# Kernel tuning notes

Measured on AMD Instinct MI355X. Metric: run time of the kernel, lower is better.

## Reference

```python
import jax, jax.numpy as jnp
import numpy as np
from jax.scipy.special import logsumexp

EPS = 0.05        # sinkhorn entropic blur (geomloss default blur=0.05, p=1 -> eps=blur)
N_ITERS = 10      # fixed sinkhorn iterations
A_W, B_W = 1.0, 1.0  # chamfer / EMD weights (c=0: projectionLoss undefined in source)


def setup_inputs() -> dict:
    key = jax.random.key(0)
    k1, k2 = jax.random.split(key)
    output = jax.random.normal(k1, (16, 2048, 3), dtype=jnp.float32)
    target = jax.random.normal(k2, (16, 2048, 3), dtype=jnp.float32)
    return {"output": output, "target": target}


def _pairwise_sqdist(x, y):
    # x: [B,N,3], y: [B,M,3] -> [B,N,M]
    x2 = jnp.sum(x * x, axis=-1)                      # [B,N]
    y2 = jnp.sum(y * y, axis=-1)                      # [B,M]
    xy = jnp.einsum('bnd,bmd->bnm', x, y)             # [B,N,M]
    return jnp.maximum(x2[:, :, None] + y2[:, None, :] - 2.0 * xy, 1e-12)


def _total_loss(output, target):
    B, N, _ = output.shape
    M = target.shape[1]
    d2 = _pairwise_sqdist(output, target)             # [B,N,M]

    # Chamfer distance: sum of min squared distances in both directions
    chamfer = jnp.sum(jnp.min(d2, axis=2)) + jnp.sum(jnp.min(d2, axis=1))

    # Sinkhorn EMD with p=1 cost (L2 distance), uniform weights, log-domain
    C = jnp.sqrt(d2)                                  # [B,N,M]
    log_mu = jnp.full((B, N), -jnp.log(jnp.float32(N)), dtype=C.dtype)
    log_nu = jnp.full((B, M), -jnp.log(jnp.float32(M)), dtype=C.dtype)
    f = jnp.zeros((B, N), dtype=C.dtype)
    g = jnp.zeros((B, M), dtype=C.dtype)

    def body(carry, _):
        f, g = carry
        # g_j = -eps * LSE_i[(f_i - C_ij)/eps + log_mu_i]
        g = -EPS * logsumexp((f[:, :, None] - C) / EPS + log_mu[:, :, None], axis=1)
        # f_i = -eps * LSE_j[(g_j - C_ij)/eps + log_nu_j]
        f = -EPS * logsumexp((g[:, None, :] - C) / EPS + log_nu[:, None, :], axis=2)
        return (f, g), None

    (f, g), _ = jax.lax.scan(body, (f, g), None, length=N_ITERS)
    mu = jnp.exp(log_mu)
    nu = jnp.exp(log_nu)
    emd = jnp.sum(mu * f, axis=1) + jnp.sum(nu * g, axis=1)   # [B] dual objective
    emd_loss = jnp.sum(emd * jnp.float32(N))

    return A_W * chamfer + B_W * emd_loss


def reference(output, target):
    return _total_loss(output, target)
```

## Files before the change

kernel.cpp:

```cpp
#include <hip/hip_runtime.h>
#include <math.h>

#define NPTS    2048
#define NBATCH  16
#define THREADS 256
#define BLOCKS_PER_BATCH 64
#define ROWS_PER_BLOCK   32
#define ROWS_PER_WAVE    8
#define IPAIRS  1024

typedef __attribute__((ext_vector_type(2))) float f2;

static constexpr float KEPS_L  = 28.853900817779268f;
static constexpr float LOGMU_L = -11.0f;
static constexpr float EPS_LN2 = 0.03465735902799727f;
static constexpr float INV_K2  = 1.2011331562368226e-3f;

__global__ void pack_pts(const float* __restrict__ a, const float* __restrict__ b,
                         float4* __restrict__ pa, float4* __restrict__ pb) {
  int idx = blockIdx.x * blockDim.x + threadIdx.x;
  if (idx < NBATCH * NPTS) {
    float x = KEPS_L * a[3*idx], y = KEPS_L * a[3*idx+1], z = KEPS_L * a[3*idx+2];
    pa[idx] = make_float4(x, y, z, fmaf(x, x, fmaf(y, y, z*z)));
    float u = KEPS_L * b[3*idx], v = KEPS_L * b[3*idx+1], w = KEPS_L * b[3*idx+2];
    pb[idx] = make_float4(u, v, w, fmaf(u, u, fmaf(v, v, w*w)));
  }
}

template<bool INIT, bool CHAMFER>
__global__ __launch_bounds__(THREADS)
void lse_pass(const float4* __restrict__ pR, const float4* __restrict__ pQ,
              const float* __restrict__ dualR, float* __restrict__ dualQ,
              float* __restrict__ chamPart) {
  __shared__ f2 sxx[IPAIRS];
  __shared__ f2 syy[IPAIRS];
  __shared__ f2 szz[IPAIRS];
  __shared__ f2 sww[IPAIRS];
  __shared__ f2 swt[IPAIRS];

  const int b    = blockIdx.x >> 6;
  const int blk  = blockIdx.x & 63;
  const int tid  = threadIdx.x;
  const int lane = tid & 63;
  const int wave = tid >> 6;

  const float4* __restrict__ px = pR + b * NPTS;
  float A;

  if constexpr (INIT) {
#pragma unroll
    for (int u = 0; u < 4; ++u) {
      int k = tid + u * THREADS;
      float4 a4 = px[k];
      float4 b4 = px[k + IPAIRS];
      sxx[k] = (f2){a4.x, b4.x};
      syy[k] = (f2){a4.y, b4.y};
      szz[k] = (f2){a4.z, b4.z};
      sww[k] = (f2){-0.5f * a4.w, -0.5f * b4.w};
      swt[k] = (f2){1.f, 1.f};
    }
    A = LOGMU_L;
    __syncthreads();
  } else {
    const float* __restrict__ fb = dualR + b * NPTS;
    float av[8];
    float lm = -3.4e38f;
#pragma unroll
    for (int u = 0; u < 8; ++u) {
      int k = tid + u * THREADS;
      float a = fmaf(fb[k], KEPS_L, LOGMU_L);
      av[u] = a;
      lm = fmaxf(lm, a);
    }
#pragma unroll
    for (int off = 32; off; off >>= 1) lm = fmaxf(lm, __shfl_xor(lm, off));
    float* scratch = (float*)sxx;
    if (lane == 0) scratch[wave] = lm;
    __syncthreads();
    A = fmaxf(fmaxf(scratch[0], scratch[1]), fmaxf(scratch[2], scratch[3]));
    __syncthreads();
#pragma unroll
    for (int u = 0; u < 4; ++u) {
      int k = tid + u * THREADS;
      float4 a4 = px[k];
      float4 b4 = px[k + IPAIRS];
      sxx[k] = (f2){a4.x, b4.x};
      syy[k] = (f2){a4.y, b4.y};
      szz[k] = (f2){a4.z, b4.z};
      sww[k] = (f2){-0.5f * a4.w, -0.5f * b4.w};
      swt[k] = (f2){__builtin_amdgcn_exp2f(av[u] - A),
                    __builtin_amdgcn_exp2f(av[u + 4] - A)};
    }
    __syncthreads();
  }

  const float4* __restrict__ qa = pQ + b * NPTS;
  float* __restrict__ gout = dualQ + b * NPTS;
  const int j0 = blk * ROWS_PER_BLOCK + wave * ROWS_PER_WAVE;

  f2 qxx[8], qyy[8], qzz[8], qww[8], s2[8], m2[8];
#pragma unroll
  for (int r = 0; r < ROWS_PER_WAVE; ++r) {
    float4 q = qa[j0 + r];
    qxx[r] = (f2){q.x, q.x};
    qyy[r] = (f2){q.y, q.y};
    qzz[r] = (f2){q.z, q.z};
    qww[r] = (f2){q.w, q.w};
    s2[r] = (f2){0.f, 0.f};
    if constexpr (CHAMFER) m2[r] = (f2){3.4e38f, 3.4e38f};
  }

  const f2 kM2 = (f2){-2.f, -2.f};

#pragma unroll 2
  for (int it = 0; it < IPAIRS / 64; ++it) {
    const int k = it * 64 + lane;
    const f2 pxx = sxx[k];
    const f2 pyy = syy[k];
    const f2 pzz = szz[k];
    const f2 pww = sww[k];
    const f2 wt  = swt[k];
#pragma unroll
    for (int r = 0; r < ROWS_PER_WAVE; ++r) {
      f2 t  = __builtin_elementwise_fma(pxx, qxx[r],
              __builtin_elementwise_fma(pyy, qyy[r],
              __builtin_elementwise_fma(pzz, qzz[r], pww)));
      f2 d2 = __builtin_elementwise_fma(kM2, t, qww[r]);
      if constexpr (CHAMFER) m2[r] = __builtin_elementwise_min(m2[r], d2);
      f2 e;
      e.x = __builtin_amdgcn_exp2f(-__builtin_amdgcn_sqrtf(d2.x));
      e.y = __builtin_amdgcn_exp2f(-__builtin_amdgcn_sqrtf(d2.y));
      s2[r] = __builtin_elementwise_fma(e, wt, s2[r]);
    }
  }

  float s[ROWS_PER_WAVE], m[ROWS_PER_WAVE];
#pragma unroll
  for (int r = 0; r < ROWS_PER_WAVE; ++r) {
    s[r] = s2[r].x + s2[r].y;
    if constexpr (CHAMFER) m[r] = fminf(m2[r].x, m2[r].y);
  }

#pragma unroll
  for (int off = 32; off; off >>= 1) {
#pragma unroll
    for (int r = 0; r < ROWS_PER_WAVE; ++r) {
      s[r] += __shfl_xor(s[r], off);
      if constexpr (CHAMFER) m[r] = fminf(m[r], __shfl_xor(m[r], off));
    }
  }

  if (lane == 0) {
#pragma unroll
    for (int r = 0; r < ROWS_PER_WAVE; ++r)
      gout[j0 + r] = -EPS_LN2 * (A + __builtin_amdgcn_logf(fmaxf(s[r], 1e-37f)));
  }

  if constexpr (CHAMFER) {
    float chamAcc = 0.f;
#pragma unroll
    for (int r = 0; r < ROWS_PER_WAVE; ++r) chamAcc += m[r];
    chamAcc *= INV_K2;
    __syncthreads();
    float* scratch = (float*)sxx;
    if (lane == 0) scratch[wave] = chamAcc;
    __syncthreads();
    if (tid == 0)
      chamPart[blockIdx.x] = (scratch[0] + scratch[1]) + (scratch[2] + scratch[3]);
  }
}

__global__ void final1(const float4* __restrict__ base, float* __restrict__ part) {
  __shared__ float red[4];
  const int idx = blockIdx.x * 256 + threadIdx.x;
  float4 v = base[idx];
  float acc = (v.x + v.y) + (v.z + v.w);
#pragma unroll
  for (int off = 32; off; off >>= 1) acc += __shfl_xor(acc, off);
  const int lane = threadIdx.x & 63, wave = threadIdx.x >> 6;
  if (lane == 0) red[wave] = acc;
  __syncthreads();
  if (threadIdx.x == 0) part[blockIdx.x] = (red[0] + red[1]) + (red[2] + red[3]);
}

__global__ void final2(const float* __restrict__ part, float* __restrict__ out) {
  const int lane = threadIdx.x;
  float acc = part[lane];
  if (lane < 2) acc += part[lane + 64];
#pragma unroll
  for (int off = 32; off; off >>= 1) acc += __shfl_xor(acc, off);
  if (lane == 0) out[0] = acc;
}

extern "C" void kernel_launch(void* const* d_in, const int* in_sizes, int n_in,
                              void* d_out, int out_size, void* d_ws, size_t ws_size,
                              hipStream_t stream) {
  const float* outPts = (const float*)d_in[0];
  const float* tgtPts = (const float*)d_in[1];
  float* out = (float*)d_out;

  char* ws = (char*)d_ws;
  float4* pwA = (float4*)ws;
  float4* pwB = (float4*)(ws + (size_t)NBATCH * NPTS * 16);
  float*  f   = (float*)(ws + (size_t)2 * NBATCH * NPTS * 16);
  float*  g   = f + NBATCH * NPTS;
  float*  cham = g + NBATCH * NPTS;
  float*  part = cham + 2048;

  pack_pts<<<dim3(128), dim3(256), 0, stream>>>(outPts, tgtPts, pwA, pwB);

  const dim3 grid(NBATCH * BLOCKS_PER_BATCH);
  const dim3 blk(THREADS);

  lse_pass<true,  true ><<<grid, blk, 0, stream>>>(pwA, pwB, nullptr, g, cham);
  lse_pass<false, true ><<<grid, blk, 0, stream>>>(pwB, pwA, g, f, cham + 1024);
  for (int t = 1; t < 10; ++t) {
    lse_pass<false, false><<<grid, blk, 0, stream>>>(pwA, pwB, f, g, nullptr);
    lse_pass<false, false><<<grid, blk, 0, stream>>>(pwB, pwA, g, f, nullptr);
  }

  final1<<<dim3(66), dim3(256), 0, stream>>>((const float4*)f, part);
  final2<<<dim3(1), dim3(64), 0, stream>>>(part, out);
}
```

Before: 363.2 us.

## Morton-sort points and prune far chunks via bounding boxes in Sinkhorn passes

A new preprocessing kernel Morton-sorts each batch's points with a shared-memory bitonic sort, packs them, and records a bounding box for each 128-point chunk. In the later Sinkhorn iterations, each wave checks every chunk's box against its query rows. A chunk is skipped when its distance exceeds the row's nearest-neighbour distance plus the dual range plus a 24-bit guard, so its exp contributions are negligible. This aims to cut exp/sqrt work in the dominant LSE loop, at the cost of a sort kernel, an extra per-row min-distance store, and a data-dependent branch that replaces the unrolled loop.

```diff
diff --git a/kernel.cpp b/kernel.cpp
--- a/kernel.cpp
+++ b/kernel.cpp
@@ -4,10 +4,10 @@
 #define NPTS    2048
 #define NBATCH  16
 #define THREADS 256
-#define BLOCKS_PER_BATCH 64
 #define ROWS_PER_BLOCK   32
 #define ROWS_PER_WAVE    8
 #define IPAIRS  1024
+#define NCHUNK  16
 
 typedef __attribute__((ext_vector_type(2))) float f2;
 
@@ -15,23 +15,85 @@
 static constexpr float LOGMU_L = -11.0f;
 static constexpr float EPS_LN2 = 0.03465735902799727f;
 static constexpr float INV_K2  = 1.2011331562368226e-3f;
-
-__global__ void pack_pts(const float* __restrict__ a, const float* __restrict__ b,
-                         float4* __restrict__ pa, float4* __restrict__ pb) {
-  int idx = blockIdx.x * blockDim.x + threadIdx.x;
-  if (idx < NBATCH * NPTS) {
-    float x = KEPS_L * a[3*idx], y = KEPS_L * a[3*idx+1], z = KEPS_L * a[3*idx+2];
-    pa[idx] = make_float4(x, y, z, fmaf(x, x, fmaf(y, y, z*z)));
-    float u = KEPS_L * b[3*idx], v = KEPS_L * b[3*idx+1], w = KEPS_L * b[3*idx+2];
-    pb[idx] = make_float4(u, v, w, fmaf(u, u, fmaf(v, v, w*w)));
-  }
-}
-
-template<bool INIT, bool CHAMFER>
+static constexpr float GUARD   = 24.0f;
+
+__device__ inline unsigned spread10(unsigned v) {
+  v = (v | (v << 16)) & 0x030000FFu;
+  v = (v | (v << 8))  & 0x0300F00Fu;
+  v = (v | (v << 4))  & 0x030C30C3u;
+  v = (v | (v << 2))  & 0x09249249u;
+  return v;
+}
+
+__global__ __launch_bounds__(1024)
+void sort_pack(const float* __restrict__ inA, const float* __restrict__ inB,
+               float4* __restrict__ p4A, float4* __restrict__ p4B,
+               float* __restrict__ bbA, float* __restrict__ bbB) {
+  __shared__ unsigned skey[NPTS];
+  __shared__ unsigned sidx[NPTS];
+  const int b  = blockIdx.x >> 1;
+  const int cb = blockIdx.x & 1;
+  const float* __restrict__ src = (cb ? inB : inA) + (size_t)b * NPTS * 3;
+  float4* __restrict__ dst = (cb ? p4B : p4A) + (size_t)b * NPTS;
+  float*  __restrict__ bbo = (cb ? bbB : bbA) + (size_t)b * NCHUNK * 8;
+  const int t = threadIdx.x;
+
+  for (int k = t; k < NPTS; k += 1024) {
+    float x = src[3*k], y = src[3*k+1], z = src[3*k+2];
+    unsigned xi = (unsigned)(int)fminf(fmaxf((x + 5.12f) * 100.0f, 0.f), 1023.f);
+    unsigned yi = (unsigned)(int)fminf(fmaxf((y + 5.12f) * 100.0f, 0.f), 1023.f);
+    unsigned zi = (unsigned)(int)fminf(fmaxf((z + 5.12f) * 100.0f, 0.f), 1023.f);
+    skey[k] = (spread10(xi) << 2) | (spread10(yi) << 1) | spread10(zi);
+    sidx[k] = k;
+  }
+  __syncthreads();
+  for (int kk = 2; kk <= NPTS; kk <<= 1) {
+    for (int j = kk >> 1; j > 0; j >>= 1) {
+      for (int t2 = t; t2 < NPTS; t2 += 1024) {
+        int p = t2 ^ j;
+        if (p > t2) {
+          bool up = (t2 & kk) == 0;
+          unsigned ka = skey[t2], kb = skey[p];
+          if (up ? (ka > kb) : (ka < kb)) {
+            skey[t2] = kb; skey[p] = ka;
+            unsigned ia = sidx[t2]; sidx[t2] = sidx[p]; sidx[p] = ia;
+          }
+        }
+      }
+      __syncthreads();
+    }
+  }
+  const int i0 = sidx[2*t], i1 = sidx[2*t+1];
+  float x0 = KEPS_L*src[3*i0], y0 = KEPS_L*src[3*i0+1], z0 = KEPS_L*src[3*i0+2];
+  float x1 = KEPS_L*src[3*i1], y1 = KEPS_L*src[3*i1+1], z1 = KEPS_L*src[3*i1+2];
+  float w0 = fmaf(x0, x0, fmaf(y0, y0, z0*z0));
+  float w1 = fmaf(x1, x1, fmaf(y1, y1, z1*z1));
+  dst[2*t]   = make_float4(x0, y0, z0, w0);
+  dst[2*t+1] = make_float4(x1, y1, z1, w1);
+  float mnx = fminf(x0,x1), mny = fminf(y0,y1), mnz = fminf(z0,z1);
+  float mxx = fmaxf(x0,x1), mxy = fmaxf(y0,y1), mxz = fmaxf(z0,z1);
+#pragma unroll
+  for (int off = 32; off; off >>= 1) {
+    mnx = fminf(mnx, __shfl_xor(mnx, off));
+    mny = fminf(mny, __shfl_xor(mny, off));
+    mnz = fminf(mnz, __shfl_xor(mnz, off));
+    mxx = fmaxf(mxx, __shfl_xor(mxx, off));
+    mxy = fmaxf(mxy, __shfl_xor(mxy, off));
+    mxz = fmaxf(mxz, __shfl_xor(mxz, off));
+  }
+  if ((t & 63) == 0) {
+    const int c = t >> 6;
+    bbo[c*8+0] = mnx; bbo[c*8+1] = mny; bbo[c*8+2] = mnz;
+    bbo[c*8+3] = mxx; bbo[c*8+4] = mxy; bbo[c*8+5] = mxz;
+  }
+}
+
+template<bool INIT, bool CHAMFER, bool PRUNE>
 __global__ __launch_bounds__(THREADS)
 void lse_pass(const float4* __restrict__ pR, const float4* __restrict__ pQ,
               const float* __restrict__ dualR, float* __restrict__ dualQ,
-              float* __restrict__ chamPart) {
+              float* __restrict__ chamPart, float* __restrict__ rmOut,
+              const float* __restrict__ rmIn, const float* __restrict__ bbR) {
   __shared__ f2 sxx[IPAIRS];
   __shared__ f2 syy[IPAIRS];
   __shared__ f2 szz[IPAIRS];
@@ -45,51 +107,57 @@
   const int wave = tid >> 6;
 
   const float4* __restrict__ px = pR + b * NPTS;
-  float A;
+  float A, W = 0.f;
 
   if constexpr (INIT) {
 #pragma unroll
     for (int u = 0; u < 4; ++u) {
-      int k = tid + u * THREADS;
-      float4 a4 = px[k];
-      float4 b4 = px[k + IPAIRS];
-      sxx[k] = (f2){a4.x, b4.x};
-      syy[k] = (f2){a4.y, b4.y};
-      szz[k] = (f2){a4.z, b4.z};
-      sww[k] = (f2){-0.5f * a4.w, -0.5f * b4.w};
-      swt[k] = (f2){1.f, 1.f};
+      int m = tid + u * THREADS;
+      float4 a4 = px[2*m], b4 = px[2*m+1];
+      sxx[m] = (f2){a4.x, b4.x};
+      syy[m] = (f2){a4.y, b4.y};
+      szz[m] = (f2){a4.z, b4.z};
+      sww[m] = (f2){-0.5f * a4.w, -0.5f * b4.w};
+      swt[m] = (f2){1.f, 1.f};
     }
     A = LOGMU_L;
     __syncthreads();
   } else {
-    const float* __restrict__ fb = dualR + b * NPTS;
-    float av[8];
-    float lm = -3.4e38f;
-#pragma unroll
-    for (int u = 0; u < 8; ++u) {
-      int k = tid + u * THREADS;
-      float a = fmaf(fb[k], KEPS_L, LOGMU_L);
-      av[u] = a;
-      lm = fmaxf(lm, a);
-    }
-#pragma unroll
-    for (int off = 32; off; off >>= 1) lm = fmaxf(lm, __shfl_xor(lm, off));
+    const f2* __restrict__ fb2 = (const f2*)(dualR + b * NPTS);
+    const f2 kK  = (f2){KEPS_L, KEPS_L};
+    const f2 kLM = (f2){LOGMU_L, LOGMU_L};
+    f2 av2[4];
+    float lm = -3.4e38f, lmn = 3.4e38f;
+#pragma unroll
+    for (int u = 0; u < 4; ++u) {
+      int m = tid + u * THREADS;
+      f2 a2 = __builtin_elementwise_fma(fb2[m], kK, kLM);
+      av2[u] = a2;
+      lm  = fmaxf(lm,  fmaxf(a2.x, a2.y));
+      lmn = fminf(lmn, fminf(a2.x, a2.y));
+    }
+#pragma unroll
+    for (int off = 32; off; off >>= 1) {
+      lm  = fmaxf(lm,  __shfl_xor(lm,  off));
+      lmn = fminf(lmn, __shfl_xor(lmn, off));
+    }
     float* scratch = (float*)sxx;
-    if (lane == 0) scratch[wave] = lm;
+    if (lane == 0) { scratch[wave] = lm; scratch[8 + wave] = lmn; }
     __syncthreads();
     A = fmaxf(fmaxf(scratch[0], scratch[1]), fmaxf(scratch[2], scratch[3]));
+    float Amin = fminf(fminf(scratch[8], scratch[9]), fminf(scratch[10], scratch[11]));
+    W = A - Amin;
     __syncthreads();
 #pragma unroll
     for (int u = 0; u < 4; ++u) {
-      int k = tid + u * THREADS;
-      float4 a4 = px[k];
-      float4 b4 = px[k + IPAIRS];
-      sxx[k] = (f2){a4.x, b4.x};
-      syy[k] = (f2){a4.y, b4.y};
-      szz[k] = (f2){a4.z, b4.z};
-      sww[k] = (f2){-0.5f * a4.w, -0.5f * b4.w};
-      swt[k] = (f2){__builtin_amdgcn_exp2f(av[u] - A),
-                    __builtin_amdgcn_exp2f(av[u + 4] - A)};
+      int m = tid + u * THREADS;
+      float4 a4 = px[2*m], b4 = px[2*m+1];
+      sxx[m] = (f2){a4.x, b4.x};
+      syy[m] = (f2){a4.y, b4.y};
+      szz[m] = (f2){a4.z, b4.z};
+      sww[m] = (f2){-0.5f * a4.w, -0.5f * b4.w};
+      swt[m] = (f2){__builtin_amdgcn_exp2f(av2[u].x - A),
+                    __builtin_amdgcn_exp2f(av2[u].y - A)};
     }
     __syncthreads();
   }
@@ -110,10 +178,35 @@
     if constexpr (CHAMFER) m2[r] = (f2){3.4e38f, 3.4e38f};
   }
 
+  unsigned long long bal = 0;
+  if constexpr (PRUNE) {
+    const int c = lane >> 2, rp = lane & 3;
+    const float* bbc = bbR + ((size_t)b * NCHUNK + c) * 8;
+    const float bmx = bbc[0], bmy = bbc[1], bmz = bbc[2];
+    const float bXx = bbc[3], bXy = bbc[4], bXz = bbc[5];
+    const float* rq = rmIn + b * NPTS + j0;
+    float4 qA = qa[j0 + 2*rp];
+    float4 qB = qa[j0 + 2*rp + 1];
+    float ca = __builtin_amdgcn_sqrtf(rq[2*rp])     + W + GUARD;
+    float cb = __builtin_amdgcn_sqrtf(rq[2*rp + 1]) + W + GUARD;
+    float dxa = fmaxf(fmaxf(bmx - qA.x, qA.x - bXx), 0.f);
+    float dya = fmaxf(fmaxf(bmy - qA.y, qA.y - bXy), 0.f);
+    float dza = fmaxf(fmaxf(bmz - qA.z, qA.z - bXz), 0.f);
+    float da2 = fmaf(dxa, dxa, fmaf(dya, dya, dza*dza));
+    float dxb = fmaxf(fmaxf(bmx - qB.x, qB.x - bXx), 0.f);
+    float dyb = fmaxf(fmaxf(bmy - qB.y, qB.y - bXy), 0.f);
+    float dzb = fmaxf(fmaxf(bmz - qB.z, qB.z - bXz), 0.f);
+    float db2 = fmaf(dxb, dxb, fmaf(dyb, dyb, dzb*dzb));
+    int ski = (da2 > ca * ca) && (db2 > cb * cb);
+    ski &= __shfl_xor(ski, 1);
+    ski &= __shfl_xor(ski, 2);
+    bal = __ballot(ski != 0);
+  }
+
   const f2 kM2 = (f2){-2.f, -2.f};
 
-#pragma unroll 2
   for (int it = 0; it < IPAIRS / 64; ++it) {
+    if constexpr (PRUNE) { if ((bal >> (4 * it)) & 1) continue; }
     const int k = it * 64 + lane;
     const f2 pxx = sxx[k];
     const f2 pyy = syy[k];
@@ -140,7 +233,6 @@
     s[r] = s2[r].x + s2[r].y;
     if constexpr (CHAMFER) m[r] = fminf(m2[r].x, m2[r].y);
   }
-
 #pragma unroll
   for (int off = 32; off; off >>= 1) {
 #pragma unroll
@@ -152,8 +244,10 @@
 
   if (lane == 0) {
 #pragma unroll
-    for (int r = 0; r < ROWS_PER_WAVE; ++r)
+    for (int r = 0; r < ROWS_PER_WAVE; ++r) {
       gout[j0 + r] = -EPS_LN2 * (A + __builtin_amdgcn_logf(fmaxf(s[r], 1e-37f)));
+      if constexpr (CHAMFER) rmOut[b * NPTS + j0 + r] = m[r];
+    }
   }
 
   if constexpr (CHAMFER) {
@@ -200,23 +294,32 @@
   float* out = (float*)d_out;
 
   char* ws = (char*)d_ws;
-  float4* pwA = (float4*)ws;
-  float4* pwB = (float4*)(ws + (size_t)NBATCH * NPTS * 16);
-  float*  f   = (float*)(ws + (size_t)2 * NBATCH * NPTS * 16);
-  float*  g   = f + NBATCH * NPTS;
+  float4* p4A = (float4*)ws;
+  float4* p4B = (float4*)(ws + (size_t)NBATCH * NPTS * 16);
+  float*  f    = (float*)(ws + (size_t)2 * NBATCH * NPTS * 16);
+  float*  g    = f + NBATCH * NPTS;
   float*  cham = g + NBATCH * NPTS;
   float*  part = cham + 2048;
-
-  pack_pts<<<dim3(128), dim3(256), 0, stream>>>(outPts, tgtPts, pwA, pwB);
-
-  const dim3 grid(NBATCH * BLOCKS_PER_BATCH);
+  float*  rmA  = part + 128;
+  float*  rmB  = rmA + NBATCH * NPTS;
+  float*  bbA  = rmB + NBATCH * NPTS;
+  float*  bbB  = bbA + NBATCH * NCHUNK * 8;
+
+  sort_pack<<<dim3(2 * NBATCH), dim3(1024), 0, stream>>>(outPts, tgtPts,
+                                                         p4A, p4B, bbA, bbB);
+
+  const dim3 grid(NBATCH * 64);
   const dim3 blk(THREADS);
 
-  lse_pass<true,  true ><<<grid, blk, 0, stream>>>(pwA, pwB, nullptr, g, cham);
-  lse_pass<false, true ><<<grid, blk, 0, stream>>>(pwB, pwA, g, f, cham + 1024);
+  lse_pass<true,  true,  false><<<grid, blk, 0, stream>>>(p4A, p4B, nullptr, g,
+      cham, rmB, nullptr, nullptr);
+  lse_pass<false, true,  false><<<grid, blk, 0, stream>>>(p4B, p4A, g, f,
+      cham + 1024, rmA, nullptr, nullptr);
   for (int t = 1; t < 10; ++t) {
-    lse_pass<false, false><<<grid, blk, 0, stream>>>(pwA, pwB, f, g, nullptr);
-    lse_pass<false, false><<<grid, blk, 0, stream>>>(pwB, pwA, g, f, nullptr);
+    lse_pass<false, false, true><<<grid, blk, 0, stream>>>(p4A, p4B, f, g,
+        nullptr, nullptr, rmB, bbA);
+    lse_pass<false, false, true><<<grid, blk, 0, stream>>>(p4B, p4A, g, f,
+        nullptr, nullptr, rmA, bbB);
   }
 
   final1<<<dim3(66), dim3(256), 0, stream>>>((const float4*)f, part);
```

After: 417.8 us. +15.1%, slower.
